# Kernel optimization log

Hardware: AMD Instinct MI355X
Metric: run time of the kernel (lower is better)

Reference implementation:

```python
import jax, jax.numpy as jnp
import numpy as np

LAMBDA_TEMP = 20.0
GAMMA = 20.0
MARGIN = 0.05
EPS = 1e-8

B, K, M, D = 128, 256, 8, 128


def _unit(x, axis=-1):
    return x / jnp.linalg.norm(x, axis=axis, keepdims=True)


def setup_inputs() -> dict:
    key = jax.random.key(0)
    k1, k2, k3 = jax.random.split(key, 3)
    v_proj = _unit(jax.random.normal(k1, (B, K, D), dtype=jnp.float32))
    prototypes = _unit(jax.random.normal(k2, (K, M, D), dtype=jnp.float32))
    concept_labels = jax.random.randint(k3, (B, K), 0, 2, dtype=jnp.int64)
    return {"v_proj": v_proj, "concept_labels": concept_labels, "prototypes": prototypes}


def reference(v_proj, concept_labels, prototypes):
    # all-pairs prototype similarities: query vector (b,k) vs prototypes of concept c
    # sims: (B, K, C, M)
    sims = jnp.einsum('bkd,cmd->bkcm', v_proj, prototypes)
    # Eq.6: soft assignment over the M prototypes of each concept
    q = jax.nn.softmax(GAMMA * sims, axis=-1)
    # Eq.7-8: weighted similarity sim_c(v)  -> (B, K, C)
    sim = jnp.sum(q * sims, axis=-1)
    # positive similarity: concept k queried against its own prototypes, plus margin
    sim_pos = jnp.einsum('bkk->bk', sim) + MARGIN  # (B, K)
    # Eq.9: -log( exp(lam*sim_pos) / (sum_c exp(lam*sim_c) + eps) )
    denom = jnp.sum(jnp.exp(LAMBDA_TEMP * sim), axis=-1) + EPS  # (B, K)
    loss_bk = jnp.log(denom) - LAMBDA_TEMP * sim_pos  # (B, K)
    mask = (concept_labels == 1).astype(loss_bk.dtype)
    num_pos = jnp.sum(mask)
    total = jnp.sum(loss_bk * mask)
    return jnp.where(num_pos > 0, total / num_pos, total)
```

## Files before the change

kernel.cpp:

```cpp
#include <hip/hip_runtime.h>

#define LT     20.0f
#define C2EXP  28.853900817779268f
#define CHUNKS 16
#define NBLK   512

typedef _Float16 half8 __attribute__((ext_vector_type(8)));
typedef float    f32x4 __attribute__((ext_vector_type(4)));

#if __has_builtin(__builtin_amdgcn_exp2f)
#define EXP2F(x) __builtin_amdgcn_exp2f(x)
#else
#define EXP2F(x) __expf(0.69314718055994531f * (x))
#endif

__device__ __forceinline__ float swz16(float x) {
    return __int_as_float(__builtin_amdgcn_ds_swizzle(__float_as_int(x), 0x401F));
}

#define GLD16(gp, lp) __builtin_amdgcn_global_load_lds( \
    (const __attribute__((address_space(1))) void*)(gp), \
    (__attribute__((address_space(3))) void*)(lp), 16, 0, 0)

__global__ __launch_bounds__(256)
void mpcl_prep(const float* __restrict__ P, _Float16* __restrict__ Pw,
               int* __restrict__ ws)
{
    int id = blockIdx.x * 256 + threadIdx.x;
    if (id == 0) ws[0] = 0;
    int ch    = id >> 11;
    int colq  = (id >> 9) & 3;
    int cfrag = (id >> 6) & 7;
    int lane  = id & 63;
    int n = lane & 15, q = lane >> 4;
    int c = cfrag & 3, h = cfrag >> 2;
    int col  = colq * 32 + ((n >> 2) << 3) + (n & 3) + (h << 2);
    int gcol = (ch << 7) + col;
    const float* src = P + ((size_t)gcol << 7) + c * 32 + q * 8;
    float4 a = *(const float4*)src;
    float4 b = *(const float4*)(src + 4);
    half8 hv;
    hv[0] = (_Float16)a.x; hv[1] = (_Float16)a.y;
    hv[2] = (_Float16)a.z; hv[3] = (_Float16)a.w;
    hv[4] = (_Float16)b.x; hv[5] = (_Float16)b.y;
    hv[6] = (_Float16)b.z; hv[7] = (_Float16)b.w;
    *(half8*)(Pw + (size_t)id * 8) = hv;
}

__global__ __attribute__((amdgpu_flat_work_group_size(512, 512),
                          amdgpu_waves_per_eu(4, 4)))
void mpcl_main(const float* __restrict__ V,
               const int*   __restrict__ labels,
               const _Float16* __restrict__ Pw,
               int* __restrict__ ws,
               float* __restrict__ out)
{
    __shared__ __align__(16) _Float16 Pst[2][2048 * 8];
    __shared__ float sh_denom[64];
    __shared__ float sh_simpos[64];
    __shared__ float sh_fin[16];
    __shared__ int   sh_last;

    int*   gcnt = ws;
    float* part = (float*)((char*)ws + 256);

    const int tid  = threadIdx.x;
    const int lane = tid & 63;
    const int w    = tid >> 6;
    const int colq = w & 3;
    const int rg   = w >> 2;
    const int n    = lane & 15;
    const int q    = lane >> 4;
    const int rowbase = blockIdx.x * 64;

    if (tid < 64) { sh_denom[tid] = 0.0f; sh_simpos[tid] = 0.0f; }

    int lab = 0;
    if (tid < 64) lab = labels[rowbase + tid];

    const _Float16* gbase = Pw + (size_t)(w * 256 + lane) * 8;

#define STAGE(CH, B) do {                                       \
    const _Float16* g_ = gbase + (size_t)(CH) * 16384;          \
    _Float16* l_ = &Pst[B][(w * 256) * 8];                      \
    GLD16(g_,        l_);                                       \
    GLD16(g_ +  512, l_ +  512);                                \
    GLD16(g_ + 1024, l_ + 1024);                                \
    GLD16(g_ + 1536, l_ + 1536);                                \
} while (0)

    STAGE(0, 0);

    half8 vh[2][4];
#pragma unroll
    for (int rf = 0; rf < 2; ++rf) {
        const float* vr = V + ((size_t)(rowbase + rg * 32 + rf * 16 + n) << 7) + q * 8;
#pragma unroll
        for (int c = 0; c < 4; ++c) {
            float4 x0 = *(const float4*)(vr + c * 32);
            float4 x1 = *(const float4*)(vr + c * 32 + 4);
            vh[rf][c][0] = (_Float16)x0.x; vh[rf][c][1] = (_Float16)x0.y;
            vh[rf][c][2] = (_Float16)x0.z; vh[rf][c][3] = (_Float16)x0.w;
            vh[rf][c][4] = (_Float16)x1.x; vh[rf][c][5] = (_Float16)x1.y;
            vh[rf][c][6] = (_Float16)x1.z; vh[rf][c][7] = (_Float16)x1.w;
        }
    }

    const int rowk0 = (rowbase + rg * 32 + n) & 255;
    const int rowk1 = (rowbase + rg * 32 + 16 + n) & 255;
    const int aoff  = (colq * 512 + lane) * 8;

    float dn0 = 0.f, dn1 = 0.f;
    int cA = colq * 4 + q;

#pragma unroll 1
    for (int ch = 0; ch < CHUNKS; ++ch) {
        __syncthreads();

        if (ch + 1 < CHUNKS) STAGE(ch + 1, (ch + 1) & 1);

        const _Float16* base = &Pst[ch & 1][0];

        f32x4 acc1[2] = {{0.f,0.f,0.f,0.f},{0.f,0.f,0.f,0.f}};
        f32x4 acc2[2] = {{0.f,0.f,0.f,0.f},{0.f,0.f,0.f,0.f}};
#pragma unroll
        for (int c = 0; c < 4; ++c) {
            half8 a1 = *(const half8*)&base[aoff + c * 512];
            half8 a2 = *(const half8*)&base[aoff + c * 512 + 2048];
            acc1[0] = __builtin_amdgcn_mfma_f32_16x16x32_f16(a1, vh[0][c], acc1[0], 0, 0, 0);
            acc1[1] = __builtin_amdgcn_mfma_f32_16x16x32_f16(a1, vh[1][c], acc1[1], 0, 0, 0);
            acc2[0] = __builtin_amdgcn_mfma_f32_16x16x32_f16(a2, vh[0][c], acc2[0], 0, 0, 0);
            acc2[1] = __builtin_amdgcn_mfma_f32_16x16x32_f16(a2, vh[1][c], acc2[1], 0, 0, 0);
        }

#pragma unroll
        for (int rf = 0; rf < 2; ++rf) {
            float x0 = acc1[rf][0], x1 = acc1[rf][1], x2 = acc1[rf][2], x3 = acc1[rf][3];
            float x4 = acc2[rf][0], x5 = acc2[rf][1], x6 = acc2[rf][2], x7 = acc2[rf][3];
            float e0 = EXP2F(C2EXP * x0), e1 = EXP2F(C2EXP * x1);
            float e2 = EXP2F(C2EXP * x2), e3 = EXP2F(C2EXP * x3);
            float e4 = EXP2F(C2EXP * x4), e5 = EXP2F(C2EXP * x5);
            float e6 = EXP2F(C2EXP * x6), e7 = EXP2F(C2EXP * x7);
            float es = ((e0 + e1) + (e2 + e3)) + ((e4 + e5) + (e6 + e7));
            float ss = fmaf(e0, x0, fmaf(e1, x1, fmaf(e2, x2, e3 * x3)))
                     + fmaf(e4, x4, fmaf(e5, x5, fmaf(e6, x6, e7 * x7)));
            float simc = __fdividef(ss, es);
            if (rf) dn1 += EXP2F(C2EXP * simc); else dn0 += EXP2F(C2EXP * simc);
            if (cA == (rf ? rowk1 : rowk0))
                sh_simpos[rg * 32 + rf * 16 + n] = simc;
        }
        cA += 16;
    }

#pragma unroll
    for (int rf = 0; rf < 2; ++rf) {
        float t = rf ? dn1 : dn0;
        t += swz16(t);
        t += __shfl_xor(t, 32);
        if (lane < 16)
            atomicAdd(&sh_denom[rg * 32 + rf * 16 + n], t);
    }
    __syncthreads();

    float s = 0.f, cc = 0.f;
    if (tid < 64) {
        float lp = logf(sh_denom[tid] + 1e-8f) - LT * (sh_simpos[tid] + 0.05f);
        float mk = (lab == 1) ? 1.0f : 0.0f;
        s = lp * mk;
        cc = mk;
    }
#pragma unroll
    for (int off = 32; off >= 1; off >>= 1) {
        s  += __shfl_down(s, off);
        cc += __shfl_down(cc, off);
    }

    if (tid == 0) {
        __hip_atomic_store(&part[2 * blockIdx.x],     s,  __ATOMIC_RELAXED, __HIP_MEMORY_SCOPE_AGENT);
        __hip_atomic_store(&part[2 * blockIdx.x + 1], cc, __ATOMIC_RELAXED, __HIP_MEMORY_SCOPE_AGENT);
        __threadfence();
        int g = __hip_atomic_fetch_add(gcnt, 1, __ATOMIC_ACQ_REL, __HIP_MEMORY_SCOPE_AGENT);
        sh_last = (g == NBLK - 1);
    }
    __syncthreads();
    if (sh_last) {
        float ts = 0.f, tc = 0.f;
        for (int i = tid; i < NBLK; i += 512) {
            ts += __hip_atomic_load(&part[2 * i],     __ATOMIC_RELAXED, __HIP_MEMORY_SCOPE_AGENT);
            tc += __hip_atomic_load(&part[2 * i + 1], __ATOMIC_RELAXED, __HIP_MEMORY_SCOPE_AGENT);
        }
#pragma unroll
        for (int off = 32; off >= 1; off >>= 1) {
            ts += __shfl_down(ts, off);
            tc += __shfl_down(tc, off);
        }
        if (lane == 0) { sh_fin[w] = ts; sh_fin[8 + w] = tc; }
        __syncthreads();
        if (tid == 0) {
            ts = 0.f; tc = 0.f;
#pragma unroll
            for (int i = 0; i < 8; ++i) { ts += sh_fin[i]; tc += sh_fin[8 + i]; }
            out[0] = (tc > 0.0f) ? (ts / tc) : ts;
        }
    }
}

extern "C" void kernel_launch(void* const* d_in, const int* in_sizes, int n_in,
                              void* d_out, int out_size, void* d_ws, size_t ws_size,
                              hipStream_t stream)
{
    const float* V      = (const float*)d_in[0];
    const int*   labels = (const int*)d_in[1];
    const float* P      = (const float*)d_in[2];
    float* out = (float*)d_out;
    int*   ws  = (int*)d_ws;
    _Float16* Pw = (_Float16*)((char*)d_ws + 16384);

    mpcl_prep<<<128, 256, 0, stream>>>(P, Pw, ws);
    mpcl_main<<<NBLK, 512, 0, stream>>>(V, labels, Pw, ws, out);
}
```

Before: 108.9 us.

## Prescale prototypes by exp constant, replicate fp16 copies, deepen async LDS prefetch

Folds the softmax/exp scale into the fp16 prototype conversion, so the main loop feeds MFMA outputs straight into exp2 without extra multiplies, and adjusts the final loss formula to match. Writes eight replicated copies of the converted prototypes and has each block read the copy chosen by its block index, to spread L2/channel contention. Replaces the per-chunk syncthreads plus single-ahead staging with two-deep prefetch using explicit vmcnt waits and raw barriers. Scaling prototypes by about 28.85 before the fp16 cast costs some precision, and the prep kernel now does eight times more work.

```diff
diff --git a/kernel.cpp b/kernel.cpp
--- a/kernel.cpp
+++ b/kernel.cpp
@@ -1,9 +1,11 @@
 #include <hip/hip_runtime.h>
 
-#define LT     20.0f
-#define C2EXP  28.853900817779268f
-#define CHUNKS 16
-#define NBLK   512
+#define LT      20.0f
+#define LN2     0.69314718055994531f
+#define C2EXP   28.853900817779268f
+#define CHUNKS  16
+#define NBLK    512
+#define PW_COPY 262144
 
 typedef _Float16 half8 __attribute__((ext_vector_type(8)));
 typedef float    f32x4 __attribute__((ext_vector_type(4)));
@@ -26,8 +28,9 @@
 void mpcl_prep(const float* __restrict__ P, _Float16* __restrict__ Pw,
                int* __restrict__ ws)
 {
-    int id = blockIdx.x * 256 + threadIdx.x;
-    if (id == 0) ws[0] = 0;
+    if (blockIdx.x == 0 && threadIdx.x == 0) ws[0] = 0;
+    int copy = blockIdx.x & 7;
+    int id   = (blockIdx.x >> 3) * 256 + threadIdx.x;
     int ch    = id >> 11;
     int colq  = (id >> 9) & 3;
     int cfrag = (id >> 6) & 7;
@@ -40,11 +43,11 @@
     float4 a = *(const float4*)src;
     float4 b = *(const float4*)(src + 4);
     half8 hv;
-    hv[0] = (_Float16)a.x; hv[1] = (_Float16)a.y;
-    hv[2] = (_Float16)a.z; hv[3] = (_Float16)a.w;
-    hv[4] = (_Float16)b.x; hv[5] = (_Float16)b.y;
-    hv[6] = (_Float16)b.z; hv[7] = (_Float16)b.w;
-    *(half8*)(Pw + (size_t)id * 8) = hv;
+    hv[0] = (_Float16)(C2EXP * a.x); hv[1] = (_Float16)(C2EXP * a.y);
+    hv[2] = (_Float16)(C2EXP * a.z); hv[3] = (_Float16)(C2EXP * a.w);
+    hv[4] = (_Float16)(C2EXP * b.x); hv[5] = (_Float16)(C2EXP * b.y);
+    hv[6] = (_Float16)(C2EXP * b.z); hv[7] = (_Float16)(C2EXP * b.w);
+    *(half8*)(Pw + (size_t)copy * PW_COPY + (size_t)id * 8) = hv;
 }
 
 __global__ __attribute__((amdgpu_flat_work_group_size(512, 512),
@@ -78,7 +81,8 @@
     int lab = 0;
     if (tid < 64) lab = labels[rowbase + tid];
 
-    const _Float16* gbase = Pw + (size_t)(w * 256 + lane) * 8;
+    const _Float16* gbase = Pw + (size_t)(blockIdx.x & 7) * PW_COPY
+                               + (size_t)(w * 256 + lane) * 8;
 
 #define STAGE(CH, B) do {                                       \
     const _Float16* g_ = gbase + (size_t)(CH) * 16384;          \
@@ -89,8 +93,6 @@
     GLD16(g_ + 1536, l_ + 1536);                                \
 } while (0)
 
-    STAGE(0, 0);
-
     half8 vh[2][4];
 #pragma unroll
     for (int rf = 0; rf < 2; ++rf) {
@@ -106,6 +108,11 @@
         }
     }
 
+    __syncthreads();
+
+    STAGE(0, 0);
+    STAGE(1, 1);
+
     const int rowk0 = (rowbase + rg * 32 + n) & 255;
     const int rowk1 = (rowbase + rg * 32 + 16 + n) & 255;
     const int aoff  = (colq * 512 + lane) * 8;
@@ -115,9 +122,9 @@
 
 #pragma unroll 1
     for (int ch = 0; ch < CHUNKS; ++ch) {
-        __syncthreads();
-
-        if (ch + 1 < CHUNKS) STAGE(ch + 1, (ch + 1) & 1);
+        if (ch < CHUNKS - 1) asm volatile("s_waitcnt vmcnt(4)" ::: "memory");
+        else                 asm volatile("s_waitcnt vmcnt(0)" ::: "memory");
+        __builtin_amdgcn_s_barrier();
 
         const _Float16* base = &Pst[ch & 1][0];
 
@@ -137,19 +144,20 @@
         for (int rf = 0; rf < 2; ++rf) {
             float x0 = acc1[rf][0], x1 = acc1[rf][1], x2 = acc1[rf][2], x3 = acc1[rf][3];
             float x4 = acc2[rf][0], x5 = acc2[rf][1], x6 = acc2[rf][2], x7 = acc2[rf][3];
-            float e0 = EXP2F(C2EXP * x0), e1 = EXP2F(C2EXP * x1);
-            float e2 = EXP2F(C2EXP * x2), e3 = EXP2F(C2EXP * x3);
-            float e4 = EXP2F(C2EXP * x4), e5 = EXP2F(C2EXP * x5);
-            float e6 = EXP2F(C2EXP * x6), e7 = EXP2F(C2EXP * x7);
+            float e0 = EXP2F(x0), e1 = EXP2F(x1), e2 = EXP2F(x2), e3 = EXP2F(x3);
+            float e4 = EXP2F(x4), e5 = EXP2F(x5), e6 = EXP2F(x6), e7 = EXP2F(x7);
             float es = ((e0 + e1) + (e2 + e3)) + ((e4 + e5) + (e6 + e7));
             float ss = fmaf(e0, x0, fmaf(e1, x1, fmaf(e2, x2, e3 * x3)))
                      + fmaf(e4, x4, fmaf(e5, x5, fmaf(e6, x6, e7 * x7)));
-            float simc = __fdividef(ss, es);
-            if (rf) dn1 += EXP2F(C2EXP * simc); else dn0 += EXP2F(C2EXP * simc);
+            float simY = __fdividef(ss, es);
+            if (rf) dn1 += EXP2F(simY); else dn0 += EXP2F(simY);
             if (cA == (rf ? rowk1 : rowk0))
-                sh_simpos[rg * 32 + rf * 16 + n] = simc;
+                sh_simpos[rg * 32 + rf * 16 + n] = simY;
         }
         cA += 16;
+
+        __builtin_amdgcn_s_barrier();
+        if (ch + 2 < CHUNKS) STAGE(ch + 2, ch & 1);
     }
 
 #pragma unroll
@@ -164,7 +172,7 @@
 
     float s = 0.f, cc = 0.f;
     if (tid < 64) {
-        float lp = logf(sh_denom[tid] + 1e-8f) - LT * (sh_simpos[tid] + 0.05f);
+        float lp = logf(sh_denom[tid] + 1e-8f) - LN2 * sh_simpos[tid] - 1.0f;
         float mk = (lab == 1) ? 1.0f : 0.0f;
         s = lp * mk;
         cc = mk;
@@ -216,6 +224,6 @@
     int*   ws  = (int*)d_ws;
     _Float16* Pw = (_Float16*)((char*)d_ws + 16384);
 
-    mpcl_prep<<<128, 256, 0, stream>>>(P, Pw, ws);
+    mpcl_prep<<<1024, 256, 0, stream>>>(P, Pw, ws);
     mpcl_main<<<NBLK, 512, 0, stream>>>(V, labels, Pw, ws, out);
 }
```

Result: no change. 109.9 us (+0.9%).
